# Optimization experiments

Measured on AMD Instinct MI355X. Metric: run time of the kernel, lower is better.

## Reference

```python
import jax, jax.numpy as jnp
import numpy as np

EPS = 1e-6

def _rms_norm(x, w):
    # torch: x / (||x||_2 * n^{-1/2} + eps) * w
    rms = jnp.linalg.norm(x, axis=-1, keepdims=True) * (x.shape[-1] ** -0.5)
    return x / (rms + EPS) * w

def _rope_cos_sin(seq_len, head_dim):
    half = head_dim // 2
    freq = 1.0 / (10000.0 ** (jnp.arange(half, dtype=jnp.float32) / half))
    t = jnp.arange(seq_len, dtype=jnp.float32)
    freqs = t[:, None] * freq[None, :]            # [s, half]
    freqs = jnp.concatenate([freqs, freqs], -1)   # [s, d_head]
    cos = jnp.cos(freqs)[None, :, None, :]        # [1, s, 1, d_head]
    sin = jnp.sin(freqs)[None, :, None, :]
    return cos, sin

def _rotate_half(x):
    h = x.shape[-1] // 2
    return jnp.concatenate([-x[..., h:], x[..., :h]], -1)

def setup_inputs() -> dict:
    key = jax.random.key(0)
    ks = jax.random.split(key, 8)
    B, S, D, H, F = 2, 2048, 2048, 16, 128
    return {
        'query_input': jax.random.normal(ks[0], (B, S, D), jnp.float32),
        'key_input':   jax.random.normal(ks[1], (B, S, D), jnp.float32),
        'value_input': jax.random.normal(ks[2], (B, S, D), jnp.float32),
        'W_Q': jax.random.normal(ks[3], (H, D, F), jnp.float32) * (D ** -0.5),
        'W_K': jax.random.normal(ks[4], (H, D, F), jnp.float32) * (D ** -0.5),
        'W_V': jax.random.normal(ks[5], (H, D, F), jnp.float32) * (D ** -0.5),
        'W_O': jax.random.normal(ks[6], (H, F, D), jnp.float32) * (F ** -0.5),
        'b_Q': jnp.zeros((H, F), jnp.float32),
        'b_K': jnp.zeros((H, F), jnp.float32),
        'b_V': jnp.zeros((H, F), jnp.float32),
        'b_O': jnp.zeros((D,), jnp.float32),
        'q_norm_w': jnp.ones((F,), jnp.float32),
        'k_norm_w': jnp.ones((F,), jnp.float32),
    }

def reference(query_input, key_input, value_input, W_Q, W_K, W_V, W_O,
              b_Q, b_K, b_V, b_O, q_norm_w, k_norm_w):
    head_dim = W_Q.shape[-1]
    q = jnp.einsum('bpd,hdf->bphf', query_input, W_Q) + b_Q[None, None]
    k = jnp.einsum('bpd,hdf->bphf', key_input,   W_K) + b_K[None, None]
    v = jnp.einsum('bpd,hdf->bphf', value_input, W_V) + b_V[None, None]
    q = _rms_norm(q, q_norm_w)
    k = _rms_norm(k, k_norm_w)
    cos, sin = _rope_cos_sin(q.shape[1], head_dim)
    q = q * cos + _rotate_half(q) * sin
    k = k * cos + _rotate_half(k) * sin
    scores = jnp.einsum('bphf,bqhf->bhpq', q, k) / (head_dim ** 0.5)
    pattern = jax.nn.softmax(scores, axis=-1)
    attn = jnp.einsum('bhpq,bqhf->bphf', pattern, v)
    return jnp.einsum('bphf,hfm->bpm', attn, W_O) + b_O
```

## Files before the change

kernel.cpp:

```cpp
#include <hip/hip_runtime.h>
#include <stdint.h>

typedef unsigned short u16;
typedef __attribute__((ext_vector_type(8))) short  s8b;
typedef __attribute__((ext_vector_type(4))) float  f32x4;

#define S_LEN   2048
#define NHEAD   16
#define HD      128
#define DM      2048
#define NB      2
#define NPLANE  (NB*NHEAD)
#define ROWS    (NB*S_LEN)
#define PLANE_ELEMS (S_LEN*HD)
#define ATT_SCALE 0.08838834764831845f
#define LOG2E     1.4426950408889634f

__device__ __forceinline__ float bf2f(u16 u){
  union { unsigned u; float f; } x; x.u = ((unsigned)u) << 16; return x.f;
}
__device__ __forceinline__ u16 f2bf(float f){
  union { float f; unsigned u; } x; x.f = f;
  unsigned r = x.u + 0x7FFFu + ((x.u >> 16) & 1u);
  return (u16)(r >> 16);
}
__device__ __forceinline__ unsigned cvtpk(float lo, float hi){
  unsigned r;
  asm("v_cvt_pk_bf16_f32 %0, %1, %2" : "=v"(r) : "v"(lo), "v"(hi));
  return r;
}

typedef const __attribute__((address_space(1))) unsigned int* gas1;
typedef __attribute__((address_space(3))) unsigned int* las3;
__device__ __forceinline__ void gload16(const void* g, void* l){
  __builtin_amdgcn_global_load_lds((gas1)g, (las3)l, 16, 0, 0);
}

__device__ __forceinline__ f32x4 mfma16(s8b a, s8b b, f32x4 c){
  return __builtin_amdgcn_mfma_f32_16x16x32_bf16(a, b, c, 0, 0, 0);
}

__global__ __launch_bounds__(256) void cvt4x3(const float4* __restrict__ a,
                                              const float4* __restrict__ b,
                                              const float4* __restrict__ c,
                                              uint2* __restrict__ oa,
                                              uint2* __restrict__ ob,
                                              uint2* __restrict__ oc, int n4){
  int i = blockIdx.x*256 + threadIdx.x;
  if (i >= n4) return;
  const float4* src = (blockIdx.y == 0) ? a : (blockIdx.y == 1) ? b : c;
  uint2*       dst  = (blockIdx.y == 0) ? oa : (blockIdx.y == 1) ? ob : oc;
  float4 v = src[i];
  uint2 o;
  o.x = (unsigned)f2bf(v.x) | ((unsigned)f2bf(v.y) << 16);
  o.y = (unsigned)f2bf(v.z) | ((unsigned)f2bf(v.w) << 16);
  dst[i] = o;
}

__global__ __launch_bounds__(256) void transpose_cvt(const float* __restrict__ in,
                                                     u16* __restrict__ out,
                                                     int R, int C, int outStride){
  __shared__ float tile[32][33];
  int z = blockIdx.z;
  const float* inz = in + (size_t)z * R * C;
  u16* outz = out + (size_t)z * C * outStride;
  int r0 = blockIdx.x*32, c0 = blockIdx.y*32;
  int tx = threadIdx.x, ty = threadIdx.y;
  #pragma unroll
  for (int i=0;i<4;i++)
    tile[ty*4+i][tx] = inz[(size_t)(r0+ty*4+i)*C + c0 + tx];
  __syncthreads();
  #pragma unroll
  for (int i=0;i<4;i++)
    outz[(size_t)(c0+ty*4+i)*outStride + r0 + tx] = f2bf(tile[tx][ty*4+i]);
}

__global__ __launch_bounds__(256) void rope_tab(float* __restrict__ ctab,
                                                float* __restrict__ stab){
  int i = blockIdx.x*256 + threadIdx.x;
  int p = i >> 6, j = i & 63;
  float freq = exp2f(-(float)j * (13.287712379549449f/64.0f));
  float a = (float)p * freq;
  ctab[i] = cosf(a);
  stab[i] = sinf(a);
}

__global__ __launch_bounds__(512) void gemm_bt(const u16* __restrict__ A,
                                               const u16* __restrict__ BT,
                                               const float* __restrict__ bias,
                                               void* __restrict__ out, int mode){
  const int K = 2048;
  const int NT = 32;
  __shared__ u16 lds[6*12288];
  const int t = threadIdx.x, w = t >> 6, l = t & 63;
  const int lr = l & 15, lg = l >> 4;
  const int wr = w >> 1, wc = w & 1;
  int bid = blockIdx.x;
  int swz = (bid & 7)*32 + (bid >> 3);
  const int M0 = (swz >> 4) * 256, N0 = (swz & 15) * 128;

  f32x4 acc[4][4];
  #pragma unroll
  for (int i=0;i<4;i++)
    #pragma unroll
    for (int j=0;j<4;j++) acc[i][j] = f32x4{0.f,0.f,0.f,0.f};

  auto stageH = [&](int ttu, int h){
    int slot = (2*ttu + h) % 6;
    int tt   = ttu & 31;
    char* base = (char*)&lds[slot*12288];
    #pragma unroll
    for (int j=0;j<2;j++){
      int d = w*2048 + j*1024 + l*16;
      int row = d >> 7;
      int koff = ((l&7)*16) ^ ((row&7)<<4);
      gload16((const char*)A + ((size_t)(M0 + h*128 + row)*K + tt*64)*2 + koff,
              base + w*2048 + j*1024);
    }
    {
      int d = w*1024 + l*16;
      int row = d >> 7;
      int koff = ((l&7)*16) ^ ((row&7)<<4);
      gload16((const char*)BT + ((size_t)(N0 + h*64 + row)*K + tt*64)*2 + koff,
              base + 16384 + w*1024);
    }
  };

  stageH(0,0); stageH(0,1); stageH(1,0); stageH(1,1);

  for (int kt=0; kt<NT; kt++){
    const char* Ab = (const char*)&lds[((2*kt + (wr>>1)) % 6)*12288];
    const char* Bb = (const char*)&lds[((2*kt + wc) % 6)*12288] + 16384;

    stageH(kt+2, 0);
    asm volatile("s_waitcnt vmcnt(9)" ::: "memory");
    __builtin_amdgcn_s_barrier();
    __builtin_amdgcn_sched_barrier(0);

    s8b af[4][2];
    #pragma unroll
    for (int mi=0;mi<4;mi++)
      #pragma unroll
      for (int kc=0;kc<2;kc++){
        int rA = (wr&1)*64 + mi*16 + lr;
        af[mi][kc] = *(const s8b*)(Ab + rA*128 + ((kc*64 + lg*16) ^ ((rA&7)<<4)));
      }
    {
      s8b bf[2][2];
      #pragma unroll
      for (int nj=0;nj<2;nj++){
        int rB = nj*16 + lr;
        bf[nj][0] = *(const s8b*)(Bb + rB*128 + ((0*64 + lg*16) ^ ((rB&7)<<4)));
        bf[nj][1] = *(const s8b*)(Bb + rB*128 + ((1*64 + lg*16) ^ ((rB&7)<<4)));
      }
      __builtin_amdgcn_s_setprio(1);
      #pragma unroll
      for (int mi=0;mi<4;mi++)
        #pragma unroll
        for (int nj=0;nj<2;nj++){
          acc[mi][nj] = mfma16(af[mi][0], bf[nj][0], acc[mi][nj]);
          acc[mi][nj] = mfma16(af[mi][1], bf[nj][1], acc[mi][nj]);
        }
      __builtin_amdgcn_s_setprio(0);
    }
    stageH(kt+2, 1);
    {
      s8b bf[2][2];
      #pragma unroll
      for (int nj=0;nj<2;nj++){
        int rB = (nj+2)*16 + lr;
        bf[nj][0] = *(const s8b*)(Bb + rB*128 + ((0*64 + lg*16) ^ ((rB&7)<<4)));
        bf[nj][1] = *(const s8b*)(Bb + rB*128 + ((1*64 + lg*16) ^ ((rB&7)<<4)));
      }
      __builtin_amdgcn_s_setprio(1);
      #pragma unroll
      for (int mi=0;mi<4;mi++)
        #pragma unroll
        for (int nj=0;nj<2;nj++){
          acc[mi][nj+2] = mfma16(af[mi][0], bf[nj][0], acc[mi][nj+2]);
          acc[mi][nj+2] = mfma16(af[mi][1], bf[nj][1], acc[mi][nj+2]);
        }
      __builtin_amdgcn_s_setprio(0);
    }
    __builtin_amdgcn_sched_barrier(0);
    __builtin_amdgcn_s_barrier();
    __builtin_amdgcn_sched_barrier(0);
  }
  asm volatile("s_waitcnt vmcnt(0)" ::: "memory");

  #pragma unroll
  for (int mi=0;mi<4;mi++){
    int growb = M0 + wr*64 + mi*16 + lg*4;
    #pragma unroll
    for (int nj=0;nj<4;nj++){
      int gcol = N0 + wc*64 + nj*16 + lr;
      float bv = bias[gcol];
      #pragma unroll
      for (int r=0;r<4;r++){
        int grow = growb + r;
        float v = acc[mi][nj][r] + bv;
        if (mode == 2){
          ((float*)out)[(size_t)grow*2048 + gcol] = v;
        } else {
          int b = grow >> 11, p = grow & 2047;
          int h = gcol >> 7,  f = gcol & 127;
          if (mode == 0){
            ((u16*)out)[(((size_t)(b*NHEAD+h))*S_LEN + p)*HD + f] = f2bf(v);
          } else {
            size_t base = ((size_t)(b*NHEAD+h)*PLANE_ELEMS)*2 + (size_t)(p>>6)*16384;
            int p6 = p & 63;
            int q_ = ((p6&12)<<1) | (p6&3) | ((p6&16)>>2);
            int kvp = (p6 & 32) | q_;
            int kc = kvp >> 5, lgv = (kvp >> 3) & 3, jv = kvp & 7;
            int off = (kc*8 + (f>>4))*1024 + (lgv*16 + (f&15))*16 + jv*2;
            *(u16*)((char*)out + base + off) = f2bf(v);
          }
        }
      }
    }
  }
}

__global__ __launch_bounds__(256) void norm_rope2(const u16* __restrict__ qin,
                                                  u16* __restrict__ qout,
                                                  const float* __restrict__ qwv,
                                                  const u16* __restrict__ kin,
                                                  u16* __restrict__ kout,
                                                  const float* __restrict__ kwv,
                                                  const float* __restrict__ ctab,
                                                  const float* __restrict__ stab,
                                                  float qscale){
  int t = threadIdx.x, w = t>>6, l = t&63;
  int isK = blockIdx.y;
  const u16* in  = isK ? kin  : qin;
  u16*       outp= isK ? kout : qout;
  const float* nw= isK ? kwv  : qwv;
  float oscale   = isK ? 1.0f : qscale;
  size_t R = (size_t)blockIdx.x*4 + w;
  int p = (int)(R & (S_LEN-1));
  size_t base = R * HD;
  float x0 = bf2f(in[base + l]);
  float x1 = bf2f(in[base + 64 + l]);
  float ss = x0*x0 + x1*x1;
  #pragma unroll
  for (int m=1;m<64;m<<=1) ss += __shfl_xor(ss, m);
  float rms = sqrtf(ss * (1.0f/128.0f));
  float sc = oscale / (rms + 1e-6f);
  float xn0 = x0 * sc * nw[l];
  float xn1 = x1 * sc * nw[64+l];
  float c = ctab[(size_t)p*64 + l], s = stab[(size_t)p*64 + l];
  float o0 = xn0*c - xn1*s;
  float o1 = xn1*c + xn0*s;
  if (!isK){
    outp[base + l]      = f2bf(o0);
    outp[base + 64 + l] = f2bf(o1);
  } else {
    size_t plane = R >> 11;
    int kv = p & 63;
    size_t tb = (plane*(size_t)PLANE_ELEMS + (size_t)(p>>6)*8192) * 2;
    int b0 = (kv*256 + l*2)        ^ ((kv&7)<<4);
    int b1 = (kv*256 + (64+l)*2)   ^ ((kv&7)<<4);
    *(u16*)((char*)outp + tb + b0) = f2bf(o0);
    *(u16*)((char*)outp + tb + b1) = f2bf(o1);
  }
}

__global__ __launch_bounds__(256,2) void attn_fwd(const u16* __restrict__ qn,
                                                  const u16* __restrict__ kn,
                                                  const u16* __restrict__ vt,
                                                  u16* __restrict__ attn_out){
  __shared__ u16 Klds[4][8192];
  int t = threadIdx.x, w = t>>6, l = t&63;
  int lr = l&15, lg = l>>4;

  int bid = blockIdx.x;
  int xcd = bid & 7, j = bid >> 3;
  int plane = xcd*4 + (j >> 4);
  int qb = j & 15;
  int q0 = qb*128 + w*32;

  const s8b ones = { (short)0x3F80, (short)0x3F80, (short)0x3F80, (short)0x3F80,
                     (short)0x3F80, (short)0x3F80, (short)0x3F80, (short)0x3F80 };

  s8b qf[2][4];
  #pragma unroll
  for (int qi=0; qi<2; qi++)
    #pragma unroll
    for (int fc=0; fc<4; fc++)
      qf[qi][fc] = *(const s8b*)(qn + ((size_t)plane*S_LEN + q0 + qi*16 + lr)*HD + fc*32 + lg*8);

  f32x4 lacc[2];
  lacc[0] = f32x4{0.f,0.f,0.f,0.f};
  lacc[1] = f32x4{0.f,0.f,0.f,0.f};
  f32x4 oacc[2][8];
  #pragma unroll
  for (int qi=0;qi<2;qi++)
    #pragma unroll
    for (int i=0;i<8;i++) oacc[qi][i] = f32x4{0.f,0.f,0.f,0.f};

  const u16* kbase = kn + (size_t)plane*PLANE_ELEMS;
  const char* vbase = (const char*)vt + (size_t)plane*PLANE_ELEMS*2;

  auto stage = [&](int buf, int kt){
    #pragma unroll
    for (int i=0;i<4;i++)
      gload16(kbase + (size_t)kt*8192 + w*2048 + i*512 + l*8, &Klds[buf][w*2048 + i*512]);
  };

  auto tile = [&](int buf, int kt){
    const char* vb = vbase + (size_t)kt*16384;
    s8b vf0[8];
    #pragma unroll
    for (int fc2=0; fc2<8; fc2++)
      vf0[fc2] = *(const s8b*)(vb + fc2*1024 + l*16);

    f32x4 sacc[4][2];
    #pragma unroll
    for (int c=0;c<4;c++){
      sacc[c][0] = f32x4{0.f,0.f,0.f,0.f};
      sacc[c][1] = f32x4{0.f,0.f,0.f,0.f};
    }
    __builtin_amdgcn_s_setprio(1);
    #pragma unroll
    for (int c=0;c<4;c++){
      int kv = c*16 + lr;
      #pragma unroll
      for (int fc=0; fc<4; fc++){
        int byte = (kv*256 + (fc*32 + lg*8)*2) ^ ((kv&7)<<4);
        s8b kf = *(const s8b*)((const char*)&Klds[buf][0] + byte);
        sacc[c][0] = mfma16(kf, qf[0][fc], sacc[c][0]);
        sacc[c][1] = mfma16(kf, qf[1][fc], sacc[c][1]);
      }
    }
    __builtin_amdgcn_s_setprio(0);

    s8b vf1[8];
    #pragma unroll
    for (int fc2=0; fc2<8; fc2++)
      vf1[fc2] = *(const s8b*)(vb + (8+fc2)*1024 + l*16);

    float pv[2][4][4];
    #pragma unroll
    for (int qi=0;qi<2;qi++)
      #pragma unroll
      for (int c=0;c<4;c++){
        pv[qi][c][0] = exp2f(sacc[c][qi][0]);
        pv[qi][c][1] = exp2f(sacc[c][qi][1]);
        pv[qi][c][2] = exp2f(sacc[c][qi][2]);
        pv[qi][c][3] = exp2f(sacc[c][qi][3]);
      }

    s8b pa[2][2];
    #pragma unroll
    for (int qi=0;qi<2;qi++)
      #pragma unroll
      for (int kc=0;kc<2;kc++){
        union { s8b v; unsigned u[4]; } pu;
        pu.u[0] = cvtpk(pv[qi][2*kc][0],   pv[qi][2*kc][1]);
        pu.u[1] = cvtpk(pv[qi][2*kc][2],   pv[qi][2*kc][3]);
        pu.u[2] = cvtpk(pv[qi][2*kc+1][0], pv[qi][2*kc+1][1]);
        pu.u[3] = cvtpk(pv[qi][2*kc+1][2], pv[qi][2*kc+1][3]);
        pa[qi][kc] = pu.v;
      }

    __builtin_amdgcn_s_setprio(1);
    lacc[0] = mfma16(pa[0][0], ones, lacc[0]);
    lacc[1] = mfma16(pa[1][0], ones, lacc[1]);
    #pragma unroll
    for (int fc2=0; fc2<8; fc2++){
      oacc[0][fc2] = mfma16(pa[0][0], vf0[fc2], oacc[0][fc2]);
      oacc[1][fc2] = mfma16(pa[1][0], vf0[fc2], oacc[1][fc2]);
    }
    lacc[0] = mfma16(pa[0][1], ones, lacc[0]);
    lacc[1] = mfma16(pa[1][1], ones, lacc[1]);
    #pragma unroll
    for (int fc2=0; fc2<8; fc2++){
      oacc[0][fc2] = mfma16(pa[0][1], vf1[fc2], oacc[0][fc2]);
      oacc[1][fc2] = mfma16(pa[1][1], vf1[fc2], oacc[1][fc2]);
    }
    __builtin_amdgcn_s_setprio(0);
  };

  stage(0, 0); stage(1, 1);
  for (int it=0; it<16; it++){
    __syncthreads();
    int b0 = (2*it) & 3, b1 = (2*it+1) & 3;
    if (it < 15){
      stage((2*it+2)&3, 2*it+2);
      stage((2*it+3)&3, 2*it+3);
    }
    tile(b0, 2*it);
    tile(b1, 2*it+1);
  }

  int b = plane >> 4, h = plane & 15;
  #pragma unroll
  for (int qi=0;qi<2;qi++){
    float inv[4];
    #pragma unroll
    for (int r=0;r<4;r++) inv[r] = 1.0f / lacc[qi][r];
    #pragma unroll
    for (int fc2=0; fc2<8; fc2++){
      int f = fc2*16 + lr;
      #pragma unroll
      for (int r=0;r<4;r++){
        int row = q0 + qi*16 + lg*4 + r;
        float o = oacc[qi][fc2][r] * inv[r];
        attn_out[(((size_t)b*S_LEN + row)*NHEAD + h)*HD + f] = f2bf(o);
      }
    }
  }
}

extern "C" void kernel_launch(void* const* d_in, const int* in_sizes, int n_in,
                              void* d_out, int out_size, void* d_ws, size_t ws_size,
                              hipStream_t stream){
  const float* xq = (const float*)d_in[0];
  const float* xk = (const float*)d_in[1];
  const float* xv = (const float*)d_in[2];
  const float* WQ = (const float*)d_in[3];
  const float* WK = (const float*)d_in[4];
  const float* WV = (const float*)d_in[5];
  const float* WO = (const float*)d_in[6];
  const float* bQ = (const float*)d_in[7];
  const float* bK = (const float*)d_in[8];
  const float* bV = (const float*)d_in[9];
  const float* bO = (const float*)d_in[10];
  const float* qw = (const float*)d_in[11];
  const float* kw = (const float*)d_in[12];

  char* ws = (char*)d_ws;
  size_t off = 0;
  auto alloc = [&](size_t bytes)->void*{
    void* p = ws + off; off += (bytes + 255) & ~(size_t)255; return p;
  };
  const size_t ACT = (size_t)ROWS*DM*2;
  const size_t WMT = (size_t)DM*DM*2;
  u16* xqb  = (u16*)alloc(ACT);
  u16* xkb  = (u16*)alloc(ACT);
  u16* xvb  = (u16*)alloc(ACT);
  u16* WqT  = (u16*)alloc(WMT);
  u16* WkT  = (u16*)alloc(WMT);
  u16* WvT  = (u16*)alloc(WMT);
  u16* WoT  = (u16*)alloc(WMT);
  u16* qraw = (u16*)alloc(ACT);
  u16* kraw = (u16*)alloc(ACT);
  u16* knT  = (u16*)alloc(ACT);
  u16* vtS  = (u16*)alloc(ACT);
  u16* attn = (u16*)alloc(ACT);
  float* ctab = (float*)alloc((size_t)S_LEN*64*4);
  float* stab = (float*)alloc((size_t)S_LEN*64*4);
  if (off > ws_size) return;

  const int n4 = ROWS*DM/4;
  cvt4x3<<<dim3(n4/256, 3), dim3(256), 0, stream>>>((const float4*)xq, (const float4*)xk,
                                                    (const float4*)xv, (uint2*)xqb,
                                                    (uint2*)xkb, (uint2*)xvb, n4);
  rope_tab<<<dim3(S_LEN*64/256), dim3(256), 0, stream>>>(ctab, stab);
  transpose_cvt<<<dim3(64,4,16), dim3(32,8), 0, stream>>>(WQ, WqT, 2048, 128, 2048);
  transpose_cvt<<<dim3(64,4,16), dim3(32,8), 0, stream>>>(WK, WkT, 2048, 128, 2048);
  transpose_cvt<<<dim3(64,4,16), dim3(32,8), 0, stream>>>(WV, WvT, 2048, 128, 2048);
  transpose_cvt<<<dim3(64,64,1), dim3(32,8), 0, stream>>>(WO, WoT, 2048, 2048, 2048);

  gemm_bt<<<dim3(256), dim3(512), 0, stream>>>(xqb, WqT, bQ, qraw, 0);
  gemm_bt<<<dim3(256), dim3(512), 0, stream>>>(xkb, WkT, bK, kraw, 0);
  gemm_bt<<<dim3(256), dim3(512), 0, stream>>>(xvb, WvT, bV, vtS, 1);

  norm_rope2<<<dim3(NPLANE*S_LEN/4, 2), dim3(256), 0, stream>>>(qraw, qraw, qw,
                                                                kraw, knT, kw,
                                                                ctab, stab, ATT_SCALE*LOG2E);

  attn_fwd<<<dim3(512), dim3(256), 0, stream>>>(qraw, knT, vtS, attn);

  gemm_bt<<<dim3(256), dim3(512), 0, stream>>>(attn, WoT, bO, d_out, 2);
}
```

Before: 334.3 us.

## Shrink attention query tile, double-buffer K, merge weight transposes into one launch

The attention kernel now gives each wave 16 query rows instead of 32 and uses 64 queries per block. The grid doubles to 1024 blocks, the K staging buffer goes from four slots to two, and launch bounds allow 4 blocks per CU, all aimed at higher occupancy and better latency hiding. In exchange, each K/V tile loaded from LDS and global memory feeds half as many MFMAs, so total K and V traffic doubles. Separately, the four weight transpose launches are merged into one flat-indexed kernel to cut launch overhead.

```diff
diff --git a/kernel.cpp b/kernel.cpp
--- a/kernel.cpp
+++ b/kernel.cpp
@@ -57,15 +57,31 @@
   dst[i] = o;
 }
 
-__global__ __launch_bounds__(256) void transpose_cvt(const float* __restrict__ in,
-                                                     u16* __restrict__ out,
-                                                     int R, int C, int outStride){
+__global__ __launch_bounds__(256) void transpose_all(const float* __restrict__ WQ,
+                                                     const float* __restrict__ WK,
+                                                     const float* __restrict__ WV,
+                                                     const float* __restrict__ WO,
+                                                     u16* __restrict__ WqT,
+                                                     u16* __restrict__ WkT,
+                                                     u16* __restrict__ WvT,
+                                                     u16* __restrict__ WoT){
   __shared__ float tile[32][33];
-  int z = blockIdx.z;
+  int u = blockIdx.x;
+  int mat = u >> 12, rem = u & 4095;
+  const float* in; u16* out; int R, C, outStride, z, r0, c0;
+  if (mat == 0){
+    in = WO; out = WoT; R = 2048; C = 2048; outStride = 2048; z = 0;
+    r0 = (rem & 63)*32; c0 = (rem >> 6)*32;
+  } else {
+    in  = (mat == 1) ? WQ  : (mat == 2) ? WK  : WV;
+    out = (mat == 1) ? WqT : (mat == 2) ? WkT : WvT;
+    R = 2048; C = 128; outStride = 2048;
+    z  = rem >> 8;
+    r0 = (rem & 63)*32; c0 = ((rem >> 6) & 3)*32;
+  }
   const float* inz = in + (size_t)z * R * C;
   u16* outz = out + (size_t)z * C * outStride;
-  int r0 = blockIdx.x*32, c0 = blockIdx.y*32;
-  int tx = threadIdx.x, ty = threadIdx.y;
+  int tx = threadIdx.x & 31, ty = threadIdx.x >> 5;
   #pragma unroll
   for (int i=0;i<4;i++)
     tile[ty*4+i][tx] = inz[(size_t)(r0+ty*4+i)*C + c0 + tx];
@@ -265,38 +281,33 @@
   }
 }
 
-__global__ __launch_bounds__(256,2) void attn_fwd(const u16* __restrict__ qn,
+__global__ __launch_bounds__(256,4) void attn_fwd(const u16* __restrict__ qn,
                                                   const u16* __restrict__ kn,
                                                   const u16* __restrict__ vt,
                                                   u16* __restrict__ attn_out){
-  __shared__ u16 Klds[4][8192];
+  __shared__ u16 Klds[2][8192];
   int t = threadIdx.x, w = t>>6, l = t&63;
   int lr = l&15, lg = l>>4;
 
   int bid = blockIdx.x;
   int xcd = bid & 7, j = bid >> 3;
-  int plane = xcd*4 + (j >> 4);
-  int qb = j & 15;
-  int q0 = qb*128 + w*32;
+  int plane = xcd*4 + (j >> 5);
+  int qb = j & 31;
+  int q0 = qb*64 + w*16;
 
   const s8b ones = { (short)0x3F80, (short)0x3F80, (short)0x3F80, (short)0x3F80,
                      (short)0x3F80, (short)0x3F80, (short)0x3F80, (short)0x3F80 };
-
-  s8b qf[2][4];
-  #pragma unroll
-  for (int qi=0; qi<2; qi++)
-    #pragma unroll
-    for (int fc=0; fc<4; fc++)
-      qf[qi][fc] = *(const s8b*)(qn + ((size_t)plane*S_LEN + q0 + qi*16 + lr)*HD + fc*32 + lg*8);
-
-  f32x4 lacc[2];
-  lacc[0] = f32x4{0.f,0.f,0.f,0.f};
-  lacc[1] = f32x4{0.f,0.f,0.f,0.f};
-  f32x4 oacc[2][8];
-  #pragma unroll
-  for (int qi=0;qi<2;qi++)
-    #pragma unroll
-    for (int i=0;i<8;i++) oacc[qi][i] = f32x4{0.f,0.f,0.f,0.f};
+  const f32x4 z4 = {0.f,0.f,0.f,0.f};
+
+  s8b qf[4];
+  #pragma unroll
+  for (int fc=0; fc<4; fc++)
+    qf[fc] = *(const s8b*)(qn + ((size_t)plane*S_LEN + q0 + lr)*HD + fc*32 + lg*8);
+
+  f32x4 lacc = z4;
+  f32x4 oacc[8];
+  #pragma unroll
+  for (int i=0;i<8;i++) oacc[i] = z4;
 
   const u16* kbase = kn + (size_t)plane*PLANE_ELEMS;
   const char* vbase = (const char*)vt + (size_t)plane*PLANE_ELEMS*2;
@@ -307,29 +318,33 @@
       gload16(kbase + (size_t)kt*8192 + w*2048 + i*512 + l*8, &Klds[buf][w*2048 + i*512]);
   };
 
-  auto tile = [&](int buf, int kt){
+  stage(0, 0);
+  int cur = 0;
+  for (int kt=0; kt<32; kt++){
+    __syncthreads();
+    if (kt+1 < 32) stage(cur^1, kt+1);
+
     const char* vb = vbase + (size_t)kt*16384;
     s8b vf0[8];
     #pragma unroll
     for (int fc2=0; fc2<8; fc2++)
       vf0[fc2] = *(const s8b*)(vb + fc2*1024 + l*16);
 
-    f32x4 sacc[4][2];
-    #pragma unroll
-    for (int c=0;c<4;c++){
-      sacc[c][0] = f32x4{0.f,0.f,0.f,0.f};
-      sacc[c][1] = f32x4{0.f,0.f,0.f,0.f};
-    }
+    f32x4 sacc[4];
     __builtin_amdgcn_s_setprio(1);
     #pragma unroll
     for (int c=0;c<4;c++){
       int kv = c*16 + lr;
-      #pragma unroll
-      for (int fc=0; fc<4; fc++){
+      {
+        int byte = (kv*256 + (lg*8)*2) ^ ((kv&7)<<4);
+        s8b kf = *(const s8b*)((const char*)&Klds[cur][0] + byte);
+        sacc[c] = mfma16(kf, qf[0], z4);
+      }
+      #pragma unroll
+      for (int fc=1; fc<4; fc++){
         int byte = (kv*256 + (fc*32 + lg*8)*2) ^ ((kv&7)<<4);
-        s8b kf = *(const s8b*)((const char*)&Klds[buf][0] + byte);
-        sacc[c][0] = mfma16(kf, qf[0][fc], sacc[c][0]);
-        sacc[c][1] = mfma16(kf, qf[1][fc], sacc[c][1]);
+        s8b kf = *(const s8b*)((const char*)&Klds[cur][0] + byte);
+        sacc[c] = mfma16(kf, qf[fc], sacc[c]);
       }
     }
     __builtin_amdgcn_s_setprio(0);
@@ -339,75 +354,51 @@
     for (int fc2=0; fc2<8; fc2++)
       vf1[fc2] = *(const s8b*)(vb + (8+fc2)*1024 + l*16);
 
-    float pv[2][4][4];
-    #pragma unroll
-    for (int qi=0;qi<2;qi++)
-      #pragma unroll
-      for (int c=0;c<4;c++){
-        pv[qi][c][0] = exp2f(sacc[c][qi][0]);
-        pv[qi][c][1] = exp2f(sacc[c][qi][1]);
-        pv[qi][c][2] = exp2f(sacc[c][qi][2]);
-        pv[qi][c][3] = exp2f(sacc[c][qi][3]);
-      }
-
-    s8b pa[2][2];
-    #pragma unroll
-    for (int qi=0;qi<2;qi++)
-      #pragma unroll
-      for (int kc=0;kc<2;kc++){
-        union { s8b v; unsigned u[4]; } pu;
-        pu.u[0] = cvtpk(pv[qi][2*kc][0],   pv[qi][2*kc][1]);
-        pu.u[1] = cvtpk(pv[qi][2*kc][2],   pv[qi][2*kc][3]);
-        pu.u[2] = cvtpk(pv[qi][2*kc+1][0], pv[qi][2*kc+1][1]);
-        pu.u[3] = cvtpk(pv[qi][2*kc+1][2], pv[qi][2*kc+1][3]);
-        pa[qi][kc] = pu.v;
-      }
+    float pv[4][4];
+    #pragma unroll
+    for (int c=0;c<4;c++){
+      pv[c][0] = exp2f(sacc[c][0]);
+      pv[c][1] = exp2f(sacc[c][1]);
+      pv[c][2] = exp2f(sacc[c][2]);
+      pv[c][3] = exp2f(sacc[c][3]);
+    }
+
+    s8b pa[2];
+    #pragma unroll
+    for (int kc=0;kc<2;kc++){
+      union { s8b v; unsigned u[4]; } pu;
+      pu.u[0] = cvtpk(pv[2*kc][0],   pv[2*kc][1]);
+      pu.u[1] = cvtpk(pv[2*kc][2],   pv[2*kc][3]);
+      pu.u[2] = cvtpk(pv[2*kc+1][0], pv[2*kc+1][1]);
+      pu.u[3] = cvtpk(pv[2*kc+1][2], pv[2*kc+1][3]);
+      pa[kc] = pu.v;
+    }
 
     __builtin_amdgcn_s_setprio(1);
-    lacc[0] = mfma16(pa[0][0], ones, lacc[0]);
-    lacc[1] = mfma16(pa[1][0], ones, lacc[1]);
-    #pragma unroll
-    for (int fc2=0; fc2<8; fc2++){
-      oacc[0][fc2] = mfma16(pa[0][0], vf0[fc2], oacc[0][fc2]);
-      oacc[1][fc2] = mfma16(pa[1][0], vf0[fc2], oacc[1][fc2]);
-    }
-    lacc[0] = mfma16(pa[0][1], ones, lacc[0]);
-    lacc[1] = mfma16(pa[1][1], ones, lacc[1]);
-    #pragma unroll
-    for (int fc2=0; fc2<8; fc2++){
-      oacc[0][fc2] = mfma16(pa[0][1], vf1[fc2], oacc[0][fc2]);
-      oacc[1][fc2] = mfma16(pa[1][1], vf1[fc2], oacc[1][fc2]);
-    }
+    lacc = mfma16(pa[0], ones, lacc);
+    #pragma unroll
+    for (int fc2=0; fc2<8; fc2++)
+      oacc[fc2] = mfma16(pa[0], vf0[fc2], oacc[fc2]);
+    lacc = mfma16(pa[1], ones, lacc);
+    #pragma unroll
+    for (int fc2=0; fc2<8; fc2++)
+      oacc[fc2] = mfma16(pa[1], vf1[fc2], oacc[fc2]);
     __builtin_amdgcn_s_setprio(0);
-  };
-
-  stage(0, 0); stage(1, 1);
-  for (int it=0; it<16; it++){
-    __syncthreads();
-    int b0 = (2*it) & 3, b1 = (2*it+1) & 3;
-    if (it < 15){
-      stage((2*it+2)&3, 2*it+2);
-      stage((2*it+3)&3, 2*it+3);
-    }
-    tile(b0, 2*it);
-    tile(b1, 2*it+1);
+    cur ^= 1;
   }
 
   int b = plane >> 4, h = plane & 15;
-  #pragma unroll
-  for (int qi=0;qi<2;qi++){
-    float inv[4];
-    #pragma unroll
-    for (int r=0;r<4;r++) inv[r] = 1.0f / lacc[qi][r];
-    #pragma unroll
-    for (int fc2=0; fc2<8; fc2++){
-      int f = fc2*16 + lr;
-      #pragma unroll
-      for (int r=0;r<4;r++){
-        int row = q0 + qi*16 + lg*4 + r;
-        float o = oacc[qi][fc2][r] * inv[r];
-        attn_out[(((size_t)b*S_LEN + row)*NHEAD + h)*HD + f] = f2bf(o);
-      }
+  float inv[4];
+  #pragma unroll
+  for (int r=0;r<4;r++) inv[r] = 1.0f / lacc[r];
+  #pragma unroll
+  for (int fc2=0; fc2<8; fc2++){
+    int f = fc2*16 + lr;
+    #pragma unroll
+    for (int r=0;r<4;r++){
+      int row = q0 + lg*4 + r;
+      float o = oacc[fc2][r] * inv[r];
+      attn_out[(((size_t)b*S_LEN + row)*NHEAD + h)*HD + f] = f2bf(o);
     }
   }
 }
@@ -457,10 +448,7 @@
                                                     (const float4*)xv, (uint2*)xqb,
                                                     (uint2*)xkb, (uint2*)xvb, n4);
   rope_tab<<<dim3(S_LEN*64/256), dim3(256), 0, stream>>>(ctab, stab);
-  transpose_cvt<<<dim3(64,4,16), dim3(32,8), 0, stream>>>(WQ, WqT, 2048, 128, 2048);
-  transpose_cvt<<<dim3(64,4,16), dim3(32,8), 0, stream>>>(WK, WkT, 2048, 128, 2048);
-  transpose_cvt<<<dim3(64,4,16), dim3(32,8), 0, stream>>>(WV, WvT, 2048, 128, 2048);
-  transpose_cvt<<<dim3(64,64,1), dim3(32,8), 0, stream>>>(WO, WoT, 2048, 2048, 2048);
+  transpose_all<<<dim3(4*4096), dim3(256), 0, stream>>>(WQ, WK, WV, WO, WqT, WkT, WvT, WoT);
 
   gemm_bt<<<dim3(256), dim3(512), 0, stream>>>(xqb, WqT, bQ, qraw, 0);
   gemm_bt<<<dim3(256), dim3(512), 0, stream>>>(xkb, WkT, bK, kraw, 0);
@@ -470,7 +458,7 @@
                                                                 kraw, knT, kw,
                                                                 ctab, stab, ATT_SCALE*LOG2E);
 
-  attn_fwd<<<dim3(512), dim3(256), 0, stream>>>(qraw, knT, vtS, attn);
+  attn_fwd<<<dim3(1024), dim3(256), 0, stream>>>(qraw, knT, vtS, attn);
 
   gemm_bt<<<dim3(256), dim3(512), 0, stream>>>(attn, WoT, bO, d_out, 2);
 }
```

Result: slower. 555.1 us (+66.1%).
